# Kernel optimization log

Hardware: AMD Instinct MI355X
Metric: run time of the kernel (lower is better)

Reference implementation:

```python
import jax, jax.numpy as jnp
import numpy as np

N_THETA, N_GAMMA, HIDDEN = 16, 64, 64
SCENE_DIM, QUERY_DIM = 16, 60
B, N_OBJ = 65536, 10
N_STEPS, DT = 20, 0.01
K_THETA, K_GAMMA, K_CROSS = 1.0, 1.0, 0.5
TWO_PI = 2.0 * np.pi


def setup_inputs() -> dict:
    key = jax.random.key(0)
    ks = jax.random.split(key, 10)
    scene = jax.random.normal(ks[0], (B, N_OBJ, SCENE_DIM), jnp.float32)
    query = jax.random.normal(ks[1], (B, QUERY_DIM), jnp.float32)
    # per-sample seeded initial oscillator state (batched)
    theta_phase0 = jax.random.uniform(ks[2], (B, N_THETA), jnp.float32, 0.0, TWO_PI)
    gamma_phase0 = jax.random.uniform(ks[3], (B, N_GAMMA), jnp.float32, 0.0, TWO_PI)
    theta_freq = TWO_PI * (4.0 + 4.0 * jax.random.uniform(ks[4], (B, N_THETA), jnp.float32))   # theta band 4-8 Hz
    gamma_freq = TWO_PI * (30.0 + 50.0 * jax.random.uniform(ks[5], (B, N_GAMMA), jnp.float32))  # gamma band 30-80 Hz
    init = lambda k, shp, fan: (jax.random.normal(k, shp, jnp.float32) / np.sqrt(fan)).astype(jnp.float32)
    Ws = init(ks[6], (SCENE_DIM, N_GAMMA), SCENE_DIM)
    bs = jnp.zeros((N_GAMMA,), jnp.float32)
    Wq = init(ks[7], (QUERY_DIM, HIDDEN), QUERY_DIM)
    bq = jnp.zeros((HIDDEN,), jnp.float32)
    d_comb = N_THETA + N_GAMMA + HIDDEN  # 144
    W1 = init(ks[8], (d_comb, HIDDEN), d_comb)
    b1 = jnp.zeros((HIDDEN,), jnp.float32)
    W2 = init(ks[9], (HIDDEN, 2), HIDDEN)
    b2 = jnp.zeros((2,), jnp.float32)
    return {"scene": scene, "query": query,
            "theta_phase0": theta_phase0, "theta_freq": theta_freq,
            "gamma_phase0": gamma_phase0, "gamma_freq": gamma_freq,
            "Ws": Ws, "bs": bs, "Wq": Wq, "bq": bq,
            "W1": W1, "b1": b1, "W2": W2, "b2": b2}


def _integrate(theta_phase0, theta_amp0, theta_freq, gamma_phase0, gamma_amp0, gamma_freq):
    """Batched Euler integration of theta-gamma Kuramoto network.

    Mean-field all-to-all coupling: sum_j a_j*sin(p_j - p_i)
      = cos(p_i)*sum_j a_j*sin(p_j) - sin(p_i)*sum_j a_j*cos(p_j).
    """
    def step(carry, _):
        tp, ta, gp, ga = carry  # (B,Nt),(B,Nt),(B,Ng),(B,Ng)
        st, ct = jnp.sin(tp), jnp.cos(tp)
        sg, cg = jnp.sin(gp), jnp.cos(gp)
        # theta intra-population coupling (amplitude-weighted mean field)
        Ti = jnp.sum(ta * st, -1, keepdims=True)
        Tr = jnp.sum(ta * ct, -1, keepdims=True)
        coup_t = (Ti * ct - Tr * st) / N_THETA
        # gamma intra-population coupling
        Gi = jnp.sum(ga * sg, -1, keepdims=True)
        Gr = jnp.sum(ga * cg, -1, keepdims=True)
        coup_g = (Gi * cg - Gr * sg) / N_GAMMA
        # theta -> gamma cross-frequency phase coupling (mean theta field)
        mi = jnp.mean(st, -1, keepdims=True)
        mr = jnp.mean(ct, -1, keepdims=True)
        cross = mi * cg - mr * sg
        dtp = theta_freq + K_THETA * coup_t
        dgp = gamma_freq + K_GAMMA * coup_g + K_CROSS * cross
        dta = ta * (1.0 - ta * ta)   # Stuart-Landau amplitude dynamics
        dga = ga * (1.0 - ga * ga)
        new = (tp + DT * dtp, ta + DT * dta, gp + DT * dgp, ga + DT * dga)
        return new, None

    carry0 = (theta_phase0, theta_amp0, gamma_phase0, gamma_amp0)
    (tp, ta, gp, ga), _ = jax.lax.scan(step, carry0, None, length=N_STEPS)
    return tp, ta, gp, ga


def reference(scene, query, theta_phase0, theta_freq, gamma_phase0, gamma_freq,
              Ws, bs, Wq, bq, W1, b1, W2, b2):
    scene_flat = jnp.mean(scene, axis=1)                      # (B, D_scene)
    gamma_init = jax.nn.sigmoid(scene_flat @ Ws + bs)         # (B, n_gamma)
    gamma_amp0 = jax.lax.stop_gradient(gamma_init)            # .detach() in original
    theta_amp0 = jnp.ones_like(theta_phase0)
    _, ta, _, ga = _integrate(theta_phase0, theta_amp0, theta_freq,
                              gamma_phase0, gamma_amp0, gamma_freq)
    osc_feat = jnp.concatenate([ta, ga], axis=-1)             # (B, n_theta+n_gamma)
    q_feat = query @ Wq + bq                                  # (B, hidden)
    combined = jnp.concatenate([osc_feat, q_feat], axis=-1)   # (B, 144)
    h = jax.nn.relu(combined @ W1 + b1)
    logits = h @ W2 + b2
    return jax.nn.log_softmax(logits, axis=-1)
```

## Files before the change

kernel.cpp:

```cpp
#include <hip/hip_runtime.h>


typedef __fp16 h2_t  __attribute__((ext_vector_type(2)));
typedef __fp16 f16x8 __attribute__((ext_vector_type(8)));
typedef float  f32x4 __attribute__((ext_vector_type(4)));
typedef unsigned u32x4 __attribute__((ext_vector_type(4)));

union H2U { unsigned u; h2_t h; };
union F8  { u32x4 u; f16x8 h; };

__device__ __forceinline__ unsigned pk(float a, float b) {
    H2U v; v.h = __builtin_amdgcn_cvt_pkrtz(a, b);
    return v.u;
}
__device__ __forceinline__ h2_t uh(unsigned x) { H2U v; v.u = x; return v.h; }
__device__ __forceinline__ float dot2(h2_t a, h2_t b, float c) {
    return __builtin_amdgcn_fdot2(a, b, c, false);
}
__device__ __forceinline__ float F20(float g) {
    #pragma unroll
    for (int n = 0; n < 20; ++n) {
        float g2 = g * g;
        g = fmaf(0.01f, g * (1.0f - g2), g);
    }
    return g;
}

#define NWP 5888

__global__ void prep_kernel(const float* __restrict__ Ws,
                            const float* __restrict__ bs,
                            const float* __restrict__ Wq,
                            const float* __restrict__ bq,
                            const float* __restrict__ W1,
                            const float* __restrict__ b1,
                            const float* __restrict__ W2,
                            const float* __restrict__ b2,
                            float* __restrict__ ws) {
    unsigned* wsu = (unsigned*)ws;
    int gid = blockIdx.x * 256 + threadIdx.x;
    if (gid < 4096) {
        int j = gid >> 6, p = gid & 63;
        int k0 = 2 * p;
        float va = 0.f, vb = 0.f;
        if (p < 32) {
            va = W1[(16 + k0) * 64 + j];
            vb = W1[(17 + k0) * 64 + j];
        } else if (p < 62) {
            int d0 = k0 - 64;
            float s0 = 0.f, s1 = 0.f;
            #pragma unroll 16
            for (int c = 0; c < 64; ++c) {
                float w = W1[(80 + c) * 64 + j];
                s0 = fmaf(Wq[d0 * 64 + c], w, s0);
                s1 = fmaf(Wq[(d0 + 1) * 64 + c], w, s1);
            }
            va = s0; vb = s1;
        } else if (p == 62) {
            float acc = b1[j];
            #pragma unroll
            for (int r = 0; r < 16; ++r) acc += W1[r * 64 + j];
            #pragma unroll 16
            for (int c = 0; c < 64; ++c)
                acc = fmaf(bq[c], W1[(80 + c) * 64 + j], acc);
            va = acc; vb = 0.f;
        }
        wsu[gid] = pk(va, vb);
    } else if (gid < 4608) {
        int w = gid - 4096, dp = w >> 6, g = w & 63;
        wsu[gid] = pk(0.1f * Ws[(2 * dp) * 64 + g],
                      0.1f * Ws[(2 * dp + 1) * 64 + g]);
    } else if (gid < 5632) {
        int li = gid - 4608, i = li >> 1;
        float x0 = (float)i * 0.015625f - 4.0f;
        float F0 = F20(1.0f / (1.0f + expf(-x0)));
        if (li & 1) {
            float F1 = F20(1.0f / (1.0f + expf(-(x0 + 0.015625f))));
            ws[gid] = F1 - F0;
        } else {
            ws[gid] = F0;
        }
    } else if (gid < 5696) {
        ws[gid] = bs[gid - 5632];
    } else if (gid < 5824) {
        ws[gid] = W2[gid - 5696];
    } else if (gid < NWP) {
        ws[gid] = (gid == 5824) ? b2[0] : (gid == 5825) ? b2[1] : 0.f;
    }
}

#define W0o  0
#define WS2o 4096
#define LUTo 4608
#define BSo  5632
#define W2o  5696
#define QP   72
#define ACTW 2816

__global__ __launch_bounds__(256, 4) void fused_kernel(
    const float* __restrict__ scene,
    const float* __restrict__ query,
    const float* __restrict__ wsbuf,
    float* __restrict__ out)
{
    __shared__ unsigned lds[NWP];
    __shared__ unsigned actS[ACTW];

    const int t    = threadIdx.x;
    const int lane = t & 63;
    const int wv   = __builtin_amdgcn_readfirstlane(t) >> 6;
    const int eb   = blockIdx.x << 6;
    const unsigned* wsu = (const unsigned*)wsbuf;

    #pragma unroll
    for (int i = 0; i < 6; ++i) {
        const int chunk = wv * 6 + i;
        if (chunk < 23) {
            const int widx = (chunk << 8) | (lane << 2);
            const int src  = (widx < 4096) ? (widx ^ (((widx >> 6) & 7) << 2))
                                           : widx;
            __builtin_amdgcn_global_load_lds(
                (const __attribute__((address_space(1))) unsigned*)(wsu + src),
                (__attribute__((address_space(3))) unsigned*)&lds[chunk << 8],
                16, 0, 0);
        }
    }

    const int sel = t >> 2, q4 = t & 3;
    {
        const float4* sp = (const float4*)scene + (size_t)(eb + sel) * 40 + q4;
        float4 a = sp[0];
        #pragma unroll
        for (int o = 1; o < 10; ++o) {
            float4 v = sp[4 * o];
            a.x += v.x; a.y += v.y; a.z += v.z; a.w += v.w;
        }
        actS[((q4 << 1) + 0) * 64 + sel] = pk(a.x, a.y);
        actS[((q4 << 1) + 1) * 64 + sel] = pk(a.z, a.w);
    }
    #pragma unroll
    for (int i = 0; i < 4; ++i) {
        const int idx = t + (i << 8);
        if (idx < 960) {
            const int qel = idx / 15, kq = idx - qel * 15;
            float4 qv = ((const float4*)query)[(size_t)(eb + qel) * 15 + kq];
            actS[512 + (2 * kq + 0) * QP + qel] = pk(qv.x, qv.y);
            actS[512 + (2 * kq + 1) * QP + qel] = pk(qv.z, qv.w);
        }
    }
    if (t < 64)       actS[512 + 30 * QP + t]        = pk(1.0f, 0.0f);
    else if (t < 128) actS[512 + 31 * QP + (t - 64)] = 0u;

    __syncthreads();

    const int kb  = lane >> 4;
    const int elb = ((t >> 6) << 4) | (lane & 15);

    unsigned sf2[8];
    #pragma unroll
    for (int dp = 0; dp < 8; ++dp) sf2[dp] = actS[dp * 64 + elb];

    F8 bfrag[4];
    #pragma unroll
    for (int c = 0; c < 2; ++c) {
        float g[8];
        #pragma unroll
        for (int s = 0; s < 2; ++s) {
            unsigned wqa[8][4];
            #pragma unroll
            for (int dp = 0; dp < 8; ++dp) {
                u32x4 w = *(const u32x4*)&lds[WS2o + dp * 64 + (c << 5) + (kb << 3) + (s << 2)];
                wqa[dp][0] = w[0]; wqa[dp][1] = w[1];
                wqa[dp][2] = w[2]; wqa[dp][3] = w[3];
            }
            #pragma unroll
            for (int i2 = 0; i2 < 4; ++i2) {
                float x = __uint_as_float(lds[BSo + (c << 5) + (kb << 3) + (s << 2) + i2]);
                #pragma unroll
                for (int dp = 0; dp < 8; ++dp)
                    x = dot2(uh(sf2[dp]), uh(wqa[dp][i2]), x);
                float u = fminf(fmaxf(fmaf(x, 64.0f, 256.0f), 0.0f), 511.0f);
                int   i0 = (int)u;
                float2 e = *(const float2*)&lds[LUTo + (i0 << 1)];
                g[(s << 2) + i2] = fmaf(u - (float)i0, e.y, e.x);
            }
        }
        F8 f;
        f.u[0] = pk(g[0], g[1]); f.u[1] = pk(g[2], g[3]);
        f.u[2] = pk(g[4], g[5]); f.u[3] = pk(g[6], g[7]);
        bfrag[c] = f;
    }
    #pragma unroll
    for (int c2 = 0; c2 < 2; ++c2) {
        F8 f;
        #pragma unroll
        for (int r = 0; r < 4; ++r)
            f.u[r] = actS[512 + ((kb << 2) + r + (c2 << 4)) * QP + elb];
        bfrag[2 + c2] = f;
    }

    float l0 = 0.f, l1 = 0.f;
    #pragma unroll
    for (int jt = 0; jt < 4; ++jt) {
        f32x4 acc = {0.f, 0.f, 0.f, 0.f};
        const int j = (jt << 4) | (lane & 15);
        #pragma unroll
        for (int c = 0; c < 4; ++c) {
            const int ch = ((c << 2) | kb) ^ (j & 7);
            F8 a;
            a.u = *(const u32x4*)&lds[W0o + (j << 6) + (ch << 2)];
            acc = __builtin_amdgcn_mfma_f32_16x16x32_f16(a.h, bfrag[c].h, acc, 0, 0, 0);
        }
        #pragma unroll
        for (int r = 0; r < 4; ++r) {
            const int jr = (jt << 4) + (kb << 2) + r;
            float hv = fmaxf(acc[r], 0.f);
            float2 wv2 = *(const float2*)&lds[W2o + (jr << 1)];
            l0 = fmaf(hv, wv2.x, l0);
            l1 = fmaf(hv, wv2.y, l1);
        }
    }
    l0 += __shfl_xor(l0, 16); l0 += __shfl_xor(l0, 32);
    l1 += __shfl_xor(l1, 16); l1 += __shfl_xor(l1, 32);
    l0 += wsbuf[5824]; l1 += wsbuf[5825];
    if (lane < 16) {
        const float mx = fmaxf(l0, l1);
        const float lz = mx + __logf(__expf(l0 - mx) + __expf(l1 - mx));
        float2 o = { l0 - lz, l1 - lz };
        ((float2*)out)[eb + elb] = o;
    }
}

extern "C" void kernel_launch(void* const* d_in, const int* in_sizes, int n_in,
                              void* d_out, int out_size, void* d_ws, size_t ws_size,
                              hipStream_t stream) {
    const float* scene = (const float*)d_in[0];
    const float* query = (const float*)d_in[1];
    const float* Ws = (const float*)d_in[6];
    const float* bs = (const float*)d_in[7];
    const float* Wq = (const float*)d_in[8];
    const float* bq = (const float*)d_in[9];
    const float* W1 = (const float*)d_in[10];
    const float* b1 = (const float*)d_in[11];
    const float* W2 = (const float*)d_in[12];
    const float* b2 = (const float*)d_in[13];
    float* out = (float*)d_out;
    float* ws  = (float*)d_ws;

    const int B = in_sizes[0] / 160;
    prep_kernel<<<23, 256, 0, stream>>>(Ws, bs, Wq, bq, W1, b1, W2, b2, ws);
    fused_kernel<<<B / 64, 256, 0, stream>>>(scene, query, ws, out);
}
```

Measured before the change: 25.54 us.

## Compute scene projection with MFMA and read W1 fragments from global memory

Replaces the per-thread fdot2 scene-to-gamma projection with 16x16x16 f16 MFMA calls that use the bias as the accumulator init. The main W1 fragments are now read straight from global/L2 rather than staged into LDS, and prep reorders W1 rows so the MFMA output layout lines up with the later B fragments. LDS use falls to a single smaller array, and launch bounds rise to 5 blocks per CU to raise occupancy. The trade is that every wave now issues global loads for the W1 fragments, which depends on cache hits.

```diff
diff --git a/kernel.cpp b/kernel.cpp
--- a/kernel.cpp
+++ b/kernel.cpp
@@ -2,20 +2,18 @@
 
 
 typedef __fp16 h2_t  __attribute__((ext_vector_type(2)));
+typedef __fp16 f16x4 __attribute__((ext_vector_type(4)));
 typedef __fp16 f16x8 __attribute__((ext_vector_type(8)));
 typedef float  f32x4 __attribute__((ext_vector_type(4)));
 typedef unsigned u32x4 __attribute__((ext_vector_type(4)));
 
 union H2U { unsigned u; h2_t h; };
+union F4  { unsigned u[2]; f16x4 h; };
 union F8  { u32x4 u; f16x8 h; };
 
 __device__ __forceinline__ unsigned pk(float a, float b) {
     H2U v; v.h = __builtin_amdgcn_cvt_pkrtz(a, b);
     return v.u;
-}
-__device__ __forceinline__ h2_t uh(unsigned x) { H2U v; v.u = x; return v.h; }
-__device__ __forceinline__ float dot2(h2_t a, h2_t b, float c) {
-    return __builtin_amdgcn_fdot2(a, b, c, false);
 }
 __device__ __forceinline__ float F20(float g) {
     #pragma unroll
@@ -41,13 +39,14 @@
     int gid = blockIdx.x * 256 + threadIdx.x;
     if (gid < 4096) {
         int j = gid >> 6, p = gid & 63;
-        int k0 = 2 * p;
         float va = 0.f, vb = 0.f;
         if (p < 32) {
-            va = W1[(16 + k0) * 64 + j];
-            vb = W1[(17 + k0) * 64 + j];
+            int c = p >> 4, kb = (p >> 2) & 3, i0 = (2 * p) & 7;
+            int g0 = ((c << 1) + (i0 >> 2)) * 16 + (kb << 2) + (i0 & 3);
+            va = W1[(16 + g0) * 64 + j];
+            vb = W1[(17 + g0) * 64 + j];
         } else if (p < 62) {
-            int d0 = k0 - 64;
+            int d0 = 2 * p - 64;
             float s0 = 0.f, s1 = 0.f;
             #pragma unroll 16
             for (int c = 0; c < 64; ++c) {
@@ -89,41 +88,37 @@
     }
 }
 
-#define W0o  0
-#define WS2o 4096
-#define LUTo 4608
-#define BSo  5632
-#define W2o  5696
+#define CWS  0
+#define CLUT 512
+#define CBS  1536
+#define CW2  1600
+#define ACTo 1728
 #define QP   72
-#define ACTW 2816
-
-__global__ __launch_bounds__(256, 4) void fused_kernel(
+#define LDSW (ACTo + 512 + 32 * QP)
+
+__global__ __launch_bounds__(256, 5) void fused_kernel(
     const float* __restrict__ scene,
     const float* __restrict__ query,
     const float* __restrict__ wsbuf,
     float* __restrict__ out)
 {
-    __shared__ unsigned lds[NWP];
-    __shared__ unsigned actS[ACTW];
-
+    __shared__ __align__(16) unsigned lds[LDSW];
     const int t    = threadIdx.x;
     const int lane = t & 63;
     const int wv   = __builtin_amdgcn_readfirstlane(t) >> 6;
     const int eb   = blockIdx.x << 6;
     const unsigned* wsu = (const unsigned*)wsbuf;
-
-    #pragma unroll
-    for (int i = 0; i < 6; ++i) {
-        const int chunk = wv * 6 + i;
-        if (chunk < 23) {
-            const int widx = (chunk << 8) | (lane << 2);
-            const int src  = (widx < 4096) ? (widx ^ (((widx >> 6) & 7) << 2))
-                                           : widx;
+    const float* ldsf = (const float*)lds;
+
+    #pragma unroll
+    for (int i = 0; i < 2; ++i) {
+        const int c = wv + (i << 2);
+        if (c < 7)
             __builtin_amdgcn_global_load_lds(
-                (const __attribute__((address_space(1))) unsigned*)(wsu + src),
-                (__attribute__((address_space(3))) unsigned*)&lds[chunk << 8],
+                (const __attribute__((address_space(1))) unsigned*)
+                    (wsu + 4096 + (c << 8) + (lane << 2)),
+                (__attribute__((address_space(3))) unsigned*)&lds[c << 8],
                 16, 0, 0);
-        }
     }
 
     const int sel = t >> 2, q4 = t & 3;
@@ -135,8 +130,8 @@
             float4 v = sp[4 * o];
             a.x += v.x; a.y += v.y; a.z += v.z; a.w += v.w;
         }
-        actS[((q4 << 1) + 0) * 64 + sel] = pk(a.x, a.y);
-        actS[((q4 << 1) + 1) * 64 + sel] = pk(a.z, a.w);
+        lds[ACTo + ((q4 << 1) + 0) * 64 + sel] = pk(a.x, a.y);
+        lds[ACTo + ((q4 << 1) + 1) * 64 + sel] = pk(a.z, a.w);
     }
     #pragma unroll
     for (int i = 0; i < 4; ++i) {
@@ -144,50 +139,46 @@
         if (idx < 960) {
             const int qel = idx / 15, kq = idx - qel * 15;
             float4 qv = ((const float4*)query)[(size_t)(eb + qel) * 15 + kq];
-            actS[512 + (2 * kq + 0) * QP + qel] = pk(qv.x, qv.y);
-            actS[512 + (2 * kq + 1) * QP + qel] = pk(qv.z, qv.w);
-        }
-    }
-    if (t < 64)       actS[512 + 30 * QP + t]        = pk(1.0f, 0.0f);
-    else if (t < 128) actS[512 + 31 * QP + (t - 64)] = 0u;
+            lds[ACTo + 512 + (2 * kq + 0) * QP + qel] = pk(qv.x, qv.y);
+            lds[ACTo + 512 + (2 * kq + 1) * QP + qel] = pk(qv.z, qv.w);
+        }
+    }
+    if (t < 64)       lds[ACTo + 512 + 30 * QP + t]        = pk(1.0f, 0.0f);
+    else if (t < 128) lds[ACTo + 512 + 31 * QP + (t - 64)] = 0u;
 
     __syncthreads();
 
     const int kb  = lane >> 4;
-    const int elb = ((t >> 6) << 4) | (lane & 15);
-
-    unsigned sf2[8];
-    #pragma unroll
-    for (int dp = 0; dp < 8; ++dp) sf2[dp] = actS[dp * 64 + elb];
-
+    const int q   = lane & 15;
+    const int elb = ((t >> 6) << 4) | q;
+
+    F4 bsf;
+    bsf.u[0] = lds[ACTo + (2 * kb + 0) * 64 + elb];
+    bsf.u[1] = lds[ACTo + (2 * kb + 1) * 64 + elb];
+    f32x4 xs[4];
+    #pragma unroll
+    for (int tt = 0; tt < 4; ++tt) {
+        F4 aW;
+        aW.u[0] = lds[CWS + (2 * kb + 0) * 64 + tt * 16 + q];
+        aW.u[1] = lds[CWS + (2 * kb + 1) * 64 + tt * 16 + q];
+        f32x4 cinit = *(const f32x4*)&ldsf[CBS + tt * 16 + (kb << 2)];
+        xs[tt] = __builtin_amdgcn_mfma_f32_16x16x16f16(aW.h, bsf.h, cinit, 0, 0, 0);
+    }
+
+    auto GA = [&](float x) -> float {
+        float u = fminf(fmaxf(fmaf(x, 64.0f, 256.0f), 0.0f), 511.0f);
+        int   i0 = (int)u;
+        float2 e = *(const float2*)&ldsf[CLUT + (i0 << 1)];
+        return fmaf(u - (float)i0, e.y, e.x);
+    };
     F8 bfrag[4];
     #pragma unroll
     for (int c = 0; c < 2; ++c) {
-        float g[8];
-        #pragma unroll
-        for (int s = 0; s < 2; ++s) {
-            unsigned wqa[8][4];
-            #pragma unroll
-            for (int dp = 0; dp < 8; ++dp) {
-                u32x4 w = *(const u32x4*)&lds[WS2o + dp * 64 + (c << 5) + (kb << 3) + (s << 2)];
-                wqa[dp][0] = w[0]; wqa[dp][1] = w[1];
-                wqa[dp][2] = w[2]; wqa[dp][3] = w[3];
-            }
-            #pragma unroll
-            for (int i2 = 0; i2 < 4; ++i2) {
-                float x = __uint_as_float(lds[BSo + (c << 5) + (kb << 3) + (s << 2) + i2]);
-                #pragma unroll
-                for (int dp = 0; dp < 8; ++dp)
-                    x = dot2(uh(sf2[dp]), uh(wqa[dp][i2]), x);
-                float u = fminf(fmaxf(fmaf(x, 64.0f, 256.0f), 0.0f), 511.0f);
-                int   i0 = (int)u;
-                float2 e = *(const float2*)&lds[LUTo + (i0 << 1)];
-                g[(s << 2) + i2] = fmaf(u - (float)i0, e.y, e.x);
-            }
-        }
         F8 f;
-        f.u[0] = pk(g[0], g[1]); f.u[1] = pk(g[2], g[3]);
-        f.u[2] = pk(g[4], g[5]); f.u[3] = pk(g[6], g[7]);
+        f.u[0] = pk(GA(xs[2 * c][0]),     GA(xs[2 * c][1]));
+        f.u[1] = pk(GA(xs[2 * c][2]),     GA(xs[2 * c][3]));
+        f.u[2] = pk(GA(xs[2 * c + 1][0]), GA(xs[2 * c + 1][1]));
+        f.u[3] = pk(GA(xs[2 * c + 1][2]), GA(xs[2 * c + 1][3]));
         bfrag[c] = f;
     }
     #pragma unroll
@@ -195,27 +186,27 @@
         F8 f;
         #pragma unroll
         for (int r = 0; r < 4; ++r)
-            f.u[r] = actS[512 + ((kb << 2) + r + (c2 << 4)) * QP + elb];
+            f.u[r] = lds[ACTo + 512 + ((kb << 2) + r + (c2 << 4)) * QP + elb];
         bfrag[2 + c2] = f;
     }
 
+    const u32x4* WgG = (const u32x4*)wsu;
     float l0 = 0.f, l1 = 0.f;
     #pragma unroll
     for (int jt = 0; jt < 4; ++jt) {
         f32x4 acc = {0.f, 0.f, 0.f, 0.f};
-        const int j = (jt << 4) | (lane & 15);
+        const int j = (jt << 4) | q;
         #pragma unroll
         for (int c = 0; c < 4; ++c) {
-            const int ch = ((c << 2) | kb) ^ (j & 7);
             F8 a;
-            a.u = *(const u32x4*)&lds[W0o + (j << 6) + (ch << 2)];
+            a.u = WgG[(j << 4) + (c << 2) + kb];
             acc = __builtin_amdgcn_mfma_f32_16x16x32_f16(a.h, bfrag[c].h, acc, 0, 0, 0);
         }
         #pragma unroll
         for (int r = 0; r < 4; ++r) {
             const int jr = (jt << 4) + (kb << 2) + r;
             float hv = fmaxf(acc[r], 0.f);
-            float2 wv2 = *(const float2*)&lds[W2o + (jr << 1)];
+            float2 wv2 = *(const float2*)&ldsf[CW2 + (jr << 1)];
             l0 = fmaf(hv, wv2.x, l0);
             l1 = fmaf(hv, wv2.y, l1);
         }
```

Result: slower. 29.00 us (+13.6%).
